# Kernel tuning notes

Measured on AMD Instinct MI355X. Metric: run time of the kernel, lower is better.

## Reference

```python
import jax, jax.numpy as jnp
import numpy as np

C_EM, H_EM, C_A = 256, 8, 32
S, R = 1024, 256
LN_EPS = 1e-5
MASK_BIAS = 1e9


def setup_inputs() -> dict:
    key = jax.random.key(0)
    ks = jax.random.split(key, 8)
    sc = 0.02
    m = jax.random.normal(ks[0], (S, R, C_EM), jnp.float32)
    # binary column mask (float mask in the original; int here so it is a constant)
    mask = (jax.random.uniform(ks[1], (S, R)) < 0.9).astype(jnp.int32)
    return {
        "m": m,
        "ln_g": jnp.ones((C_EM,), jnp.float32),
        "ln_b": jnp.zeros((C_EM,), jnp.float32),
        "w_q": jax.random.normal(ks[2], (C_EM, H_EM, C_A), jnp.float32) * sc,
        "w_k": jax.random.normal(ks[3], (C_EM, C_A), jnp.float32) * sc,
        "w_v": jax.random.normal(ks[4], (C_EM, C_A), jnp.float32) * sc,
        "w_g": jax.random.normal(ks[5], (C_EM, H_EM, C_A), jnp.float32) * sc,
        "b_g": jnp.zeros((H_EM, C_A), jnp.float32),
        "w_o": jax.random.normal(ks[6], (H_EM, C_A, C_EM), jnp.float32) * sc,
        "b_o": jnp.zeros((C_EM,), jnp.float32),
        "mask": mask,
    }


def reference(m, ln_g, ln_b, w_q, w_k, w_v, w_g, b_g, w_o, b_o, mask):
    maskf = mask.astype(m.dtype)  # [s, r]
    # LayerNorm over c_em (biased variance, eps=1e-5, torch default)
    mu = jnp.mean(m, axis=-1, keepdims=True)
    var = jnp.mean((m - mu) ** 2, axis=-1, keepdims=True)
    x = (m - mu) * jax.lax.rsqrt(var + LN_EPS) * ln_g + ln_b  # [s, r, c]
    # masked mean-pool over s -> per-column query
    q_pool = jnp.sum(x * maskf[..., None], axis=-3) / (jnp.sum(maskf, axis=-2)[..., None] + 1e-10)  # [r, c]
    Q = jnp.einsum('rc,chd->rhd', q_pool, w_q) * (1.0 / np.sqrt(C_A))  # [r, h, d]
    K = jnp.einsum('src,cd->srd', x, w_k)  # [s, r, d]
    V = jnp.einsum('src,cd->srd', x, w_v)  # [s, r, d]
    G = jax.nn.sigmoid(jnp.einsum('src,chd->srhd', x, w_g) + b_g)  # [s, r, h, d]
    bias = (maskf - 1.0) * MASK_BIAS  # [s, r]
    logits = jnp.einsum('rhd,srd->srh', Q, K) + bias[..., None]  # [s, r, h]
    A = jax.nn.softmax(logits, axis=-3)  # softmax over s
    O = jnp.einsum('srh,srd->rhd', A, V)  # [r, h, d]
    out = jnp.einsum('srhd,hdc->src', O[None, :, :, :] * G, w_o) + b_o  # [s, r, c]
    return out
```

## Files before the change

### kernel.cpp

```cpp
#include <hip/hip_runtime.h>
#include <math.h>

#define S_DIM 1024
#define R_DIM 256
#define C_DIM 256
#define SCALE 0.17677669529663687f

typedef short bf16x8 __attribute__((ext_vector_type(8)));
typedef float f32x4 __attribute__((ext_vector_type(4)));

__device__ __forceinline__ float wred(float v) {
#pragma unroll
  for (int m = 32; m >= 1; m >>= 1) v += __shfl_xor(v, m, 64);
  return v;
}

__device__ __forceinline__ short f2bf(float f) {
  union { float f; unsigned u; } v;
  v.f = f;
  unsigned r = v.u + 0x7fffu + ((v.u >> 16) & 1u);
  return (short)(r >> 16);
}

__device__ __forceinline__ float bf2f(short s) {
  union { unsigned u; float f; } v;
  v.u = ((unsigned)(unsigned short)s) << 16;
  return v.f;
}

__device__ __forceinline__ float fast_sigmoid_mul(float o, float gl) {
  return o * __builtin_amdgcn_rcpf(1.f + __expf(-gl));
}

__global__ __launch_bounds__(256)
void k0_prep(const float* __restrict__ w_g, const float* __restrict__ w_o,
             const float* __restrict__ w_k, const float* __restrict__ w_v,
             short* __restrict__ wgB, short* __restrict__ woB,
             short* __restrict__ wkvB) {
  const int id = blockIdx.x * 256 + threadIdx.x;
  if (id < 16384) {
    const int which = id >> 13;
    const int s = id & 8191;
    const int n = s & 255, g = (s >> 8) & 3, kb = s >> 10;
    const float* W = which ? w_o : w_g;
    short* Out = which ? woB : wgB;
#pragma unroll
    for (int j = 0; j < 8; ++j)
      Out[(((size_t)kb * 256 + n) * 4 + g) * 8 + j] =
          f2bf(W[(size_t)(kb * 32 + g * 8 + j) * 256 + n]);
  } else {
    const int s = id - 16384;
    const int n = s & 63, g = (s >> 6) & 3, kb = s >> 8;
    const float* W = (n < 32) ? w_k : w_v;
    const int nn = n & 31;
#pragma unroll
    for (int j = 0; j < 8; ++j)
      wkvB[(((size_t)kb * 64 + n) * 4 + g) * 8 + j] =
          f2bf(W[(size_t)(kb * 32 + g * 8 + j) * 32 + nn]);
  }
}

__global__ __launch_bounds__(256, 3)
void k1_ln_kv(const float* __restrict__ mIn, const float* __restrict__ ln_g,
              const float* __restrict__ ln_b, const short* __restrict__ wkvB,
              const int* __restrict__ mask,
              float* __restrict__ mu_ws, float* __restrict__ rs_ws,
              float* __restrict__ K_ws, float* __restrict__ V_ws,
              float* __restrict__ pool_ws) {
  __shared__ __align__(16) short A_lds[2048 * 8];
  __shared__ float mask_s[64];
  __shared__ float4 poolp[4][64];
  const int r  = blockIdx.y;
  const int s0 = blockIdx.x * 64;
  const int t  = threadIdx.x;

  if (t < 64) mask_s[t] = mask[(s0 + t) * R_DIM + r] ? 1.f : 0.f;

  {
    const int rw = t >> 2;
    const int q  = t & 3;
    const size_t p = (size_t)(s0 + rw) * R_DIM + r;
    const float* src = mIn + p * C_DIM + q * 64;
    float4 xv[16];
    float sum = 0.f, ssq = 0.f;
#pragma unroll
    for (int i = 0; i < 16; ++i) {
      xv[i] = *(const float4*)(src + i * 4);
      sum += xv[i].x + xv[i].y + xv[i].z + xv[i].w;
      ssq += xv[i].x * xv[i].x + xv[i].y * xv[i].y + xv[i].z * xv[i].z +
             xv[i].w * xv[i].w;
    }
    sum += __shfl_xor(sum, 1, 64); ssq += __shfl_xor(ssq, 1, 64);
    sum += __shfl_xor(sum, 2, 64); ssq += __shfl_xor(ssq, 2, 64);
    const float mu = sum * (1.f / 256.f);
    const float var = ssq * (1.f / 256.f) - mu * mu;
    const float rs = rsqrtf(var + 1e-5f);
    if (q == 0) { mu_ws[p] = mu; rs_ws[p] = rs; }

    const int gw = rw >> 4;
    const int lf0 = rw & 15;
#pragma unroll
    for (int kh = 0; kh < 2; ++kh) {
      const int kb = 2 * q + kh;
#pragma unroll
      for (int g = 0; g < 4; ++g) {
        const int lidx = kh * 32 + g * 8;
        const float4 a0 = xv[lidx >> 2], a1 = xv[(lidx >> 2) + 1];
        const float4 g0 = *(const float4*)(ln_g + kb * 32 + g * 8);
        const float4 g1 = *(const float4*)(ln_g + kb * 32 + g * 8 + 4);
        const float4 b0 = *(const float4*)(ln_b + kb * 32 + g * 8);
        const float4 b1 = *(const float4*)(ln_b + kb * 32 + g * 8 + 4);
        bf16x8 f;
        f[0] = f2bf((a0.x - mu) * rs * g0.x + b0.x);
        f[1] = f2bf((a0.y - mu) * rs * g0.y + b0.y);
        f[2] = f2bf((a0.z - mu) * rs * g0.z + b0.z);
        f[3] = f2bf((a0.w - mu) * rs * g0.w + b0.w);
        f[4] = f2bf((a1.x - mu) * rs * g1.x + b1.x);
        f[5] = f2bf((a1.y - mu) * rs * g1.y + b1.y);
        f[6] = f2bf((a1.z - mu) * rs * g1.z + b1.z);
        f[7] = f2bf((a1.w - mu) * rs * g1.w + b1.w);
        int byte = (((gw * 8 + kb) * 64 + lf0 + g * 16) << 4) ^ (((kb >> 1) & 3) << 5);
        *(bf16x8*)((char*)A_lds + byte) = f;
      }
    }
  }
  __syncthreads();

  {
    const int w = t >> 6, l = t & 63;
    const int lm = l & 15, g = l >> 4;
    f32x4 acc[4];
#pragma unroll
    for (int ni = 0; ni < 4; ++ni) acc[ni] = (f32x4){0.f, 0.f, 0.f, 0.f};
#pragma unroll
    for (int kb = 0; kb < 8; ++kb) {
      const int byte = (((w * 8 + kb) * 64 + l) << 4) ^ (((kb >> 1) & 3) << 5);
      const bf16x8 a = *(const bf16x8*)((char*)A_lds + byte);
      bf16x8 bfr[4];
#pragma unroll
      for (int ni = 0; ni < 4; ++ni)
        bfr[ni] = *(const bf16x8*)(wkvB + (((size_t)kb * 64 + lm + ni * 16) * 4 + g) * 8);
#pragma unroll
      for (int ni = 0; ni < 4; ++ni)
        acc[ni] = __builtin_amdgcn_mfma_f32_16x16x32_bf16(a, bfr[ni], acc[ni], 0, 0, 0);
    }
#pragma unroll
    for (int ni = 0; ni < 4; ++ni) {
      const int col = lm + ni * 16;
      float* Out = (col < 32) ? K_ws : V_ws;
      const int cc = col & 31;
#pragma unroll
      for (int reg = 0; reg < 4; ++reg) {
        const int s = s0 + w * 16 + g * 4 + reg;
        Out[((size_t)s * R_DIM + r) * 32 + cc] = acc[ni][reg];
      }
    }
  }

  {
    const int lc = t & 63;
    const int wq = t >> 6;
    const int kb = lc >> 3, g2 = (lc >> 1) & 3, bh = (lc & 1) * 4;
    float4 ps = make_float4(0.f, 0.f, 0.f, 0.f);
    for (int i = 0; i < 16; ++i) {
      const int rloc = (i + lc) & 15;
      const int byte =
          ((((wq * 8 + kb) * 64 + rloc + g2 * 16) << 4) + bh * 2) ^ (((kb >> 1) & 3) << 5);
      const short4 xb = *(const short4*)((char*)A_lds + byte);
      const float mk = mask_s[wq * 16 + rloc];
      ps.x += mk * bf2f(xb.x);
      ps.y += mk * bf2f(xb.y);
      ps.z += mk * bf2f(xb.z);
      ps.w += mk * bf2f(xb.w);
    }
    poolp[wq][lc] = ps;
  }
  __syncthreads();
  if (t < 64) {
    const float4 a = poolp[0][t], b = poolp[1][t], c = poolp[2][t], d = poolp[3][t];
    atomicAdd(&pool_ws[r * C_DIM + t * 4 + 0], a.x + b.x + c.x + d.x);
    atomicAdd(&pool_ws[r * C_DIM + t * 4 + 1], a.y + b.y + c.y + d.y);
    atomicAdd(&pool_ws[r * C_DIM + t * 4 + 2], a.z + b.z + c.z + d.z);
    atomicAdd(&pool_ws[r * C_DIM + t * 4 + 3], a.w + b.w + c.w + d.w);
  }
}

__global__ __launch_bounds__(256, 2)
void k2_q(const float* __restrict__ pool_ws, const int* __restrict__ mask,
          const float* __restrict__ w_q, float* __restrict__ Q_ws) {
  __shared__ float qp[256];
  __shared__ float wsum[4];
  const int r = blockIdx.x, t = threadIdx.x;
  int cnt = 0;
  for (int s = t; s < S_DIM; s += 256) cnt += mask[s * R_DIM + r];
  float cf = wred((float)cnt);
  if ((t & 63) == 0) wsum[t >> 6] = cf;
  __syncthreads();
  const float denom = wsum[0] + wsum[1] + wsum[2] + wsum[3] + 1e-10f;
  qp[t] = pool_ws[r * C_DIM + t] / denom;
  __syncthreads();
  float acc = 0.f;
  for (int c = 0; c < 256; ++c) acc += qp[c] * w_q[c * 256 + t];
  Q_ws[r * 256 + t] = acc * SCALE;
}

__global__ __launch_bounds__(256, 2)
void k3_attn(const float* __restrict__ K_ws, const float* __restrict__ V_ws,
             const int* __restrict__ mask, const float* __restrict__ Q_ws,
             float* __restrict__ O_ws) {
  __shared__ float q[256];
  __shared__ float lg[1024 * 9];
  __shared__ float kv[256 * 36];
  __shared__ float mh[8], inv[8];
  const int r = blockIdx.x, t = threadIdx.x;
  q[t] = Q_ws[r * 256 + t];

  for (int ch = 0; ch < 4; ++ch) {
    const int sb = ch * 256;
    __syncthreads();
    for (int f = t; f < 2048; f += 256) {
      const int sl = f >> 3, dq = f & 7;
      *(float4*)(kv + sl * 36 + dq * 4) =
          *(const float4*)(K_ws + ((size_t)(sb + sl) * R_DIM + r) * 32 + dq * 4);
    }
    __syncthreads();
    float kr[32];
#pragma unroll
    for (int dq = 0; dq < 8; ++dq)
      *(float4*)(kr + dq * 4) = *(float4*)(kv + t * 36 + dq * 4);
    const float bias = mask[(sb + t) * R_DIM + r] ? 0.f : -1e9f;
#pragma unroll
    for (int h = 0; h < 8; ++h) {
      float a = 0.f;
#pragma unroll
      for (int d = 0; d < 32; ++d) a += q[h * 32 + d] * kr[d];
      lg[(sb + t) * 9 + h] = a + bias;
    }
  }
  __syncthreads();
  {
    const int h = t >> 5, l32 = t & 31;
    float mx = -INFINITY;
    for (int k = 0; k < 32; ++k) mx = fmaxf(mx, lg[(l32 + 32 * k) * 9 + h]);
#pragma unroll
    for (int mk = 16; mk >= 1; mk >>= 1) mx = fmaxf(mx, __shfl_xor(mx, mk, 64));
    float sm = 0.f;
    for (int k = 0; k < 32; ++k) sm += __expf(lg[(l32 + 32 * k) * 9 + h] - mx);
#pragma unroll
    for (int mk = 16; mk >= 1; mk >>= 1) sm += __shfl_xor(sm, mk, 64);
    if (l32 == 0) { mh[h] = mx; inv[h] = 1.f / sm; }
  }
  __syncthreads();
  for (int f = t; f < 8192; f += 256) {
    const int s = f >> 3, h = f & 7;
    lg[s * 9 + h] = __expf(lg[s * 9 + h] - mh[h]) * inv[h];
  }
  const int h = t >> 5, d = t & 31;
  float o = 0.f;
  for (int ch = 0; ch < 4; ++ch) {
    const int sb = ch * 256;
    __syncthreads();
    for (int f = t; f < 2048; f += 256) {
      const int sl = f >> 3, dq = f & 7;
      *(float4*)(kv + sl * 36 + dq * 4) =
          *(const float4*)(V_ws + ((size_t)(sb + sl) * R_DIM + r) * 32 + dq * 4);
    }
    __syncthreads();
    for (int sl = 0; sl < 256; ++sl)
      o += lg[(sb + sl) * 9 + h] * kv[sl * 36 + d];
  }
  O_ws[r * 256 + t] = o;
}

__global__ __launch_bounds__(256, 4)
void k4_mfma(const float* __restrict__ mIn, const float* __restrict__ ln_g,
             const float* __restrict__ ln_b, const float* __restrict__ mu_ws,
             const float* __restrict__ rs_ws, const short* __restrict__ wgB,
             const float* __restrict__ b_g, const float* __restrict__ O_ws,
             const short* __restrict__ woB, const float* __restrict__ b_o,
             float* __restrict__ out) {
  __shared__ __align__(16) short A_lds[2048 * 8];
  const int t = threadIdx.x;
  const int p0 = blockIdx.x * 64;
  const int r0 = p0 & 255;
  const int l = t & 63;
  const int w = t >> 6;
  const int lm = l & 15;
  const int g = l >> 4;

  {
    const int row = w * 16 + lm;
    const size_t p = (size_t)(p0 + row);
    const float mu = mu_ws[p], rs = rs_ws[p];
    const float* mrow = mIn + p * 256 + g * 8;
    const float* gp = ln_g + g * 8;
    const float* bp = ln_b + g * 8;
#pragma unroll
    for (int kb = 0; kb < 8; ++kb) {
      const float4 m0 = *(const float4*)(mrow + kb * 32);
      const float4 m1 = *(const float4*)(mrow + kb * 32 + 4);
      const float4 g0 = *(const float4*)(gp + kb * 32);
      const float4 g1 = *(const float4*)(gp + kb * 32 + 4);
      const float4 b0 = *(const float4*)(bp + kb * 32);
      const float4 b1 = *(const float4*)(bp + kb * 32 + 4);
      bf16x8 xf;
      xf[0] = f2bf((m0.x - mu) * rs * g0.x + b0.x);
      xf[1] = f2bf((m0.y - mu) * rs * g0.y + b0.y);
      xf[2] = f2bf((m0.z - mu) * rs * g0.z + b0.z);
      xf[3] = f2bf((m0.w - mu) * rs * g0.w + b0.w);
      xf[4] = f2bf((m1.x - mu) * rs * g1.x + b1.x);
      xf[5] = f2bf((m1.y - mu) * rs * g1.y + b1.y);
      xf[6] = f2bf((m1.z - mu) * rs * g1.z + b1.z);
      xf[7] = f2bf((m1.w - mu) * rs * g1.w + b1.w);
      *(bf16x8*)(A_lds + ((w * 8 + kb) * 64 + l) * 8) = xf;
    }
  }
  __syncthreads();

  const int col = w * 64 + lm;
  f32x4 acc[4][4];

#pragma unroll
  for (int ni = 0; ni < 4; ++ni) {
    const float bg = b_g[col + ni * 16];
#pragma unroll
    for (int mi = 0; mi < 4; ++mi) acc[mi][ni] = (f32x4){bg, bg, bg, bg};
  }
#pragma unroll
  for (int kb = 0; kb < 8; ++kb) {
    bf16x8 a[4], bb[4];
#pragma unroll
    for (int mi = 0; mi < 4; ++mi)
      a[mi] = *(const bf16x8*)(A_lds + ((mi * 8 + kb) * 64 + l) * 8);
#pragma unroll
    for (int ni = 0; ni < 4; ++ni)
      bb[ni] = *(const bf16x8*)(wgB + (((size_t)kb * 256 + col + ni * 16) * 4 + g) * 8);
#pragma unroll
    for (int mi = 0; mi < 4; ++mi)
#pragma unroll
      for (int ni = 0; ni < 4; ++ni)
        acc[mi][ni] = __builtin_amdgcn_mfma_f32_16x16x32_bf16(a[mi], bb[ni], acc[mi][ni], 0, 0, 0);
  }
  __syncthreads();

#pragma unroll
  for (int mi = 0; mi < 4; ++mi) {
#pragma unroll
    for (int ni = 0; ni < 4; ++ni) {
      const int c2 = col + ni * 16;
      const int kb2 = c2 >> 5, g2 = (c2 >> 3) & 3, b2 = c2 & 7;
#pragma unroll
      for (int reg = 0; reg < 4; ++reg) {
        const int row = mi * 16 + g * 4 + reg;
        const float o = O_ws[(r0 + row) * 256 + c2];
        const float tv = fast_sigmoid_mul(o, acc[mi][ni][reg]);
        const int u = (mi * 8 + kb2) * 64 + (g * 4 + reg) + g2 * 16;
        const int byte = ((u << 4) ^ (((u >> 4) & 3) << 4)) + b2 * 2;
        *(short*)((char*)A_lds + byte) = f2bf(tv);
      }
    }
  }
  __syncthreads();

#pragma unroll
  for (int ni = 0; ni < 4; ++ni) {
    const float bo = b_o[col + ni * 16];
#pragma unroll
    for (int mi = 0; mi < 4; ++mi) acc[mi][ni] = (f32x4){bo, bo, bo, bo};
  }
#pragma unroll
  for (int kb = 0; kb < 8; ++kb) {
    bf16x8 a[4], bb[4];
#pragma unroll
    for (int mi = 0; mi < 4; ++mi) {
      const int u = (mi * 8 + kb) * 64 + l;
      const int byte = (u << 4) ^ (g << 4);
      a[mi] = *(const bf16x8*)((char*)A_lds + byte);
    }
#pragma unroll
    for (int ni = 0; ni < 4; ++ni)
      bb[ni] = *(const bf16x8*)(woB + (((size_t)kb * 256 + col + ni * 16) * 4 + g) * 8);
#pragma unroll
    for (int mi = 0; mi < 4; ++mi)
#pragma unroll
      for (int ni = 0; ni < 4; ++ni)
        acc[mi][ni] = __builtin_amdgcn_mfma_f32_16x16x32_bf16(a[mi], bb[ni], acc[mi][ni], 0, 0, 0);
  }

#pragma unroll
  for (int mi = 0; mi < 4; ++mi)
#pragma unroll
    for (int ni = 0; ni < 4; ++ni)
#pragma unroll
      for (int reg = 0; reg < 4; ++reg) {
        const int row = mi * 16 + g * 4 + reg;
        out[(size_t)(p0 + row) * 256 + col + ni * 16] = acc[mi][ni][reg];
      }
}

extern "C" void kernel_launch(void* const* d_in, const int* in_sizes, int n_in,
                              void* d_out, int out_size, void* d_ws, size_t ws_size,
                              hipStream_t stream) {
  const float* mIn  = (const float*)d_in[0];
  const float* ln_g = (const float*)d_in[1];
  const float* ln_b = (const float*)d_in[2];
  const float* w_q  = (const float*)d_in[3];
  const float* w_k  = (const float*)d_in[4];
  const float* w_v  = (const float*)d_in[5];
  const float* w_g  = (const float*)d_in[6];
  const float* b_g  = (const float*)d_in[7];
  const float* w_o  = (const float*)d_in[8];
  const float* b_o  = (const float*)d_in[9];
  const int*   mask = (const int*)d_in[10];
  float* outp = (float*)d_out;

  char* ws = (char*)d_ws;
  const size_t NP = (size_t)S_DIM * R_DIM;
  float* mu_ws   = (float*)ws;
  float* rs_ws   = mu_ws + NP;
  float* K_ws    = rs_ws + NP;
  float* V_ws    = K_ws + NP * 32;
  float* pool_ws = V_ws + NP * 32;
  float* Q_ws    = pool_ws + 65536;
  float* O_ws    = Q_ws + 65536;
  short* wgB     = (short*)(O_ws + 65536);
  short* woB     = wgB + 65536;
  short* wkvB    = woB + 65536;

  hipMemsetAsync(pool_ws, 0, 65536 * sizeof(float), stream);

  k0_prep<<<72, 256, 0, stream>>>(w_g, w_o, w_k, w_v, wgB, woB, wkvB);
  k1_ln_kv<<<dim3(S_DIM / 64, R_DIM), 256, 0, stream>>>(
      mIn, ln_g, ln_b, wkvB, mask, mu_ws, rs_ws, K_ws, V_ws, pool_ws);
  k2_q<<<R_DIM, 256, 0, stream>>>(pool_ws, mask, w_q, Q_ws);
  k3_attn<<<R_DIM, 256, 0, stream>>>(K_ws, V_ws, mask, Q_ws, O_ws);
  k4_mfma<<<dim3(S_DIM * R_DIM / 64), 256, 0, stream>>>(
      mIn, ln_g, ln_b, mu_ws, rs_ws, wgB, b_g, O_ws, woB, b_o, outp);
}
```

Baseline: 381.6 us.

## Fuse Q projection into attention kernel and prefetch weights in MFMA loops

Merges the per-column Q projection kernel into the attention kernel, so the mask is loaded once into registers and reused for both the count and the bias. This removes one launch and the Q workspace round trip. In the gating/output MFMA kernel, the B-operand weight fragments are now double-buffered in registers, loading the next k-block while the current one's MFMAs issue. The extra registers may affect occupancy.

```diff
diff --git a/kernel.cpp b/kernel.cpp
--- a/kernel.cpp
+++ b/kernel.cpp
@@ -186,34 +186,32 @@
 }
 
 __global__ __launch_bounds__(256, 2)
-void k2_q(const float* __restrict__ pool_ws, const int* __restrict__ mask,
-          const float* __restrict__ w_q, float* __restrict__ Q_ws) {
+void k3_attn(const float* __restrict__ K_ws, const float* __restrict__ V_ws,
+             const int* __restrict__ mask, const float* __restrict__ pool_ws,
+             const float* __restrict__ w_q, float* __restrict__ O_ws) {
+  __shared__ float q[256];
   __shared__ float qp[256];
-  __shared__ float wsum[4];
-  const int r = blockIdx.x, t = threadIdx.x;
-  int cnt = 0;
-  for (int s = t; s < S_DIM; s += 256) cnt += mask[s * R_DIM + r];
-  float cf = wred((float)cnt);
-  if ((t & 63) == 0) wsum[t >> 6] = cf;
-  __syncthreads();
-  const float denom = wsum[0] + wsum[1] + wsum[2] + wsum[3] + 1e-10f;
-  qp[t] = pool_ws[r * C_DIM + t] / denom;
-  __syncthreads();
-  float acc = 0.f;
-  for (int c = 0; c < 256; ++c) acc += qp[c] * w_q[c * 256 + t];
-  Q_ws[r * 256 + t] = acc * SCALE;
-}
-
-__global__ __launch_bounds__(256, 2)
-void k3_attn(const float* __restrict__ K_ws, const float* __restrict__ V_ws,
-             const int* __restrict__ mask, const float* __restrict__ Q_ws,
-             float* __restrict__ O_ws) {
-  __shared__ float q[256];
   __shared__ float lg[1024 * 9];
   __shared__ float kv[256 * 36];
   __shared__ float mh[8], inv[8];
+  __shared__ float wsum[4];
   const int r = blockIdx.x, t = threadIdx.x;
-  q[t] = Q_ws[r * 256 + t];
+
+  int mk[4];
+#pragma unroll
+  for (int ch = 0; ch < 4; ++ch) mk[ch] = mask[(ch * 256 + t) * R_DIM + r];
+  float cf = wred((float)(mk[0] + mk[1] + mk[2] + mk[3]));
+  if ((t & 63) == 0) wsum[t >> 6] = cf;
+  __syncthreads();
+  const float denom = wsum[0] + wsum[1] + wsum[2] + wsum[3] + 1e-10f;
+  qp[t] = pool_ws[r * C_DIM + t] / denom;
+  __syncthreads();
+  {
+    float qa = 0.f;
+    for (int c = 0; c < 256; ++c) qa += qp[c] * w_q[c * 256 + t];
+    q[t] = qa * SCALE;
+  }
+  __syncthreads();
 
   for (int ch = 0; ch < 4; ++ch) {
     const int sb = ch * 256;
@@ -228,7 +226,7 @@
 #pragma unroll
     for (int dq = 0; dq < 8; ++dq)
       *(float4*)(kr + dq * 4) = *(float4*)(kv + t * 36 + dq * 4);
-    const float bias = mask[(sb + t) * R_DIM + r] ? 0.f : -1e9f;
+    const float bias = mk[ch] ? 0.f : -1e9f;
 #pragma unroll
     for (int h = 0; h < 8; ++h) {
       float a = 0.f;
@@ -243,11 +241,11 @@
     float mx = -INFINITY;
     for (int k = 0; k < 32; ++k) mx = fmaxf(mx, lg[(l32 + 32 * k) * 9 + h]);
 #pragma unroll
-    for (int mk = 16; mk >= 1; mk >>= 1) mx = fmaxf(mx, __shfl_xor(mx, mk, 64));
+    for (int mkk = 16; mkk >= 1; mkk >>= 1) mx = fmaxf(mx, __shfl_xor(mx, mkk, 64));
     float sm = 0.f;
     for (int k = 0; k < 32; ++k) sm += __expf(lg[(l32 + 32 * k) * 9 + h] - mx);
 #pragma unroll
-    for (int mk = 16; mk >= 1; mk >>= 1) sm += __shfl_xor(sm, mk, 64);
+    for (int mkk = 16; mkk >= 1; mkk >>= 1) sm += __shfl_xor(sm, mkk, 64);
     if (l32 == 0) { mh[h] = mx; inv[h] = 1.f / sm; }
   }
   __syncthreads();
@@ -287,6 +285,12 @@
   const int w = t >> 6;
   const int lm = l & 15;
   const int g = l >> 4;
+  const int col = w * 64 + lm;
+
+  bf16x8 bb_c[4], bb_n[4];
+#pragma unroll
+  for (int ni = 0; ni < 4; ++ni)
+    bb_c[ni] = *(const bf16x8*)(wgB + (((size_t)0 * 256 + col + ni * 16) * 4 + g) * 8);
 
   {
     const int row = w * 16 + lm;
@@ -317,7 +321,6 @@
   }
   __syncthreads();
 
-  const int col = w * 64 + lm;
   f32x4 acc[4][4];
 
 #pragma unroll
@@ -328,19 +331,28 @@
   }
 #pragma unroll
   for (int kb = 0; kb < 8; ++kb) {
-    bf16x8 a[4], bb[4];
+    bf16x8 a[4];
 #pragma unroll
     for (int mi = 0; mi < 4; ++mi)
       a[mi] = *(const bf16x8*)(A_lds + ((mi * 8 + kb) * 64 + l) * 8);
-#pragma unroll
-    for (int ni = 0; ni < 4; ++ni)
-      bb[ni] = *(const bf16x8*)(wgB + (((size_t)kb * 256 + col + ni * 16) * 4 + g) * 8);
+    if (kb < 7) {
+#pragma unroll
+      for (int ni = 0; ni < 4; ++ni)
+        bb_n[ni] = *(const bf16x8*)(wgB +
+            (((size_t)(kb + 1) * 256 + col + ni * 16) * 4 + g) * 8);
+    }
 #pragma unroll
     for (int mi = 0; mi < 4; ++mi)
 #pragma unroll
       for (int ni = 0; ni < 4; ++ni)
-        acc[mi][ni] = __builtin_amdgcn_mfma_f32_16x16x32_bf16(a[mi], bb[ni], acc[mi][ni], 0, 0, 0);
-  }
+        acc[mi][ni] = __builtin_amdgcn_mfma_f32_16x16x32_bf16(a[mi], bb_c[ni], acc[mi][ni], 0, 0, 0);
+#pragma unroll
+    for (int ni = 0; ni < 4; ++ni) bb_c[ni] = bb_n[ni];
+  }
+
+#pragma unroll
+  for (int ni = 0; ni < 4; ++ni)
+    bb_c[ni] = *(const bf16x8*)(woB + (((size_t)0 * 256 + col + ni * 16) * 4 + g) * 8);
   __syncthreads();
 
 #pragma unroll
@@ -370,21 +382,25 @@
   }
 #pragma unroll
   for (int kb = 0; kb < 8; ++kb) {
-    bf16x8 a[4], bb[4];
+    bf16x8 a[4];
 #pragma unroll
     for (int mi = 0; mi < 4; ++mi) {
       const int u = (mi * 8 + kb) * 64 + l;
-      const int byte = (u << 4) ^ (g << 4);
-      a[mi] = *(const bf16x8*)((char*)A_lds + byte);
-    }
-#pragma unroll
-    for (int ni = 0; ni < 4; ++ni)
-      bb[ni] = *(const bf16x8*)(woB + (((size_t)kb * 256 + col + ni * 16) * 4 + g) * 8);
+      a[mi] = *(const bf16x8*)((char*)A_lds + ((u << 4) ^ (g << 4)));
+    }
+    if (kb < 7) {
+#pragma unroll
+      for (int ni = 0; ni < 4; ++ni)
+        bb_n[ni] = *(const bf16x8*)(woB +
+            (((size_t)(kb + 1) * 256 + col + ni * 16) * 4 + g) * 8);
+    }
 #pragma unroll
     for (int mi = 0; mi < 4; ++mi)
 #pragma unroll
       for (int ni = 0; ni < 4; ++ni)
-        acc[mi][ni] = __builtin_amdgcn_mfma_f32_16x16x32_bf16(a[mi], bb[ni], acc[mi][ni], 0, 0, 0);
+        acc[mi][ni] = __builtin_amdgcn_mfma_f32_16x16x32_bf16(a[mi], bb_c[ni], acc[mi][ni], 0, 0, 0);
+#pragma unroll
+    for (int ni = 0; ni < 4; ++ni) bb_c[ni] = bb_n[ni];
   }
 
 #pragma unroll
@@ -421,8 +437,7 @@
   float* K_ws    = rs_ws + NP;
   float* V_ws    = K_ws + NP * 32;
   float* pool_ws = V_ws + NP * 32;
-  float* Q_ws    = pool_ws + 65536;
-  float* O_ws    = Q_ws + 65536;
+  float* O_ws    = pool_ws + 65536;
   short* wgB     = (short*)(O_ws + 65536);
   short* woB     = wgB + 65536;
   short* wkvB    = woB + 65536;
@@ -432,8 +447,7 @@
   k0_prep<<<72, 256, 0, stream>>>(w_g, w_o, w_k, w_v, wgB, woB, wkvB);
   k1_ln_kv<<<dim3(S_DIM / 64, R_DIM), 256, 0, stream>>>(
       mIn, ln_g, ln_b, wkvB, mask, mu_ws, rs_ws, K_ws, V_ws, pool_ws);
-  k2_q<<<R_DIM, 256, 0, stream>>>(pool_ws, mask, w_q, Q_ws);
-  k3_attn<<<R_DIM, 256, 0, stream>>>(K_ws, V_ws, mask, Q_ws, O_ws);
+  k3_attn<<<R_DIM, 256, 0, stream>>>(K_ws, V_ws, mask, pool_ws, w_q, O_ws);
   k4_mfma<<<dim3(S_DIM * R_DIM / 64), 256, 0, stream>>>(
       mIn, ln_g, ln_b, mu_ws, rs_ws, wgB, b_g, O_ws, woB, b_o, outp);
 }
```

After: 395.9 us. 3.8% more time.

## Split column attention into parallel logits, AV and normalize kernels with bf16 K/V

Applied to the files above, without the earlier changes.

Replaces the single per-column attention kernel, which had only 256 blocks, with three kernels. One computes exp(logits) over a grid spread along s and column and accumulates softmax denominators with atomics. One computes partial AV products per 256-row chunk, and one sums the partials and normalizes. K and V are now written by the LN kernel as bf16 in a column-major [r][s][d] layout to halve traffic and make per-column reads contiguous. The softmax drops max subtraction, which risks overflow for large logits, and adds an exp-score buffer plus extra launches.

```diff
diff --git a/kernel.cpp b/kernel.cpp
--- a/kernel.cpp
+++ b/kernel.cpp
@@ -65,7 +65,7 @@
               const float* __restrict__ ln_b, const short* __restrict__ wkvB,
               const int* __restrict__ mask,
               float* __restrict__ mu_ws, float* __restrict__ rs_ws,
-              float* __restrict__ K_ws, float* __restrict__ V_ws,
+              short* __restrict__ Kt, short* __restrict__ Vt,
               float* __restrict__ pool_ws) {
   __shared__ __align__(16) short A_lds[2048 * 8];
   __shared__ float mask_s[64];
@@ -147,12 +147,12 @@
 #pragma unroll
     for (int ni = 0; ni < 4; ++ni) {
       const int col = lm + ni * 16;
-      float* Out = (col < 32) ? K_ws : V_ws;
+      short* Out = (col < 32) ? Kt : Vt;
       const int cc = col & 31;
 #pragma unroll
       for (int reg = 0; reg < 4; ++reg) {
         const int s = s0 + w * 16 + g * 4 + reg;
-        Out[((size_t)s * R_DIM + r) * 32 + cc] = acc[ni][reg];
+        Out[((size_t)r * 1024 + s) * 32 + cc] = f2bf(acc[ni][reg]);
       }
     }
   }
@@ -204,72 +204,83 @@
   Q_ws[r * 256 + t] = acc * SCALE;
 }
 
-__global__ __launch_bounds__(256, 2)
-void k3_attn(const float* __restrict__ K_ws, const float* __restrict__ V_ws,
-             const int* __restrict__ mask, const float* __restrict__ Q_ws,
-             float* __restrict__ O_ws) {
+__global__ __launch_bounds__(256, 4)
+void k3e_logits(const short* __restrict__ Kt, const float* __restrict__ Q_ws,
+                const int* __restrict__ mask, float* __restrict__ E_ws,
+                float* __restrict__ D_ws) {
   __shared__ float q[256];
-  __shared__ float lg[1024 * 9];
-  __shared__ float kv[256 * 36];
-  __shared__ float mh[8], inv[8];
+  const int r = blockIdx.y, s0 = blockIdx.x * 64;
+  const int t = threadIdx.x, w = t >> 6, l = t & 63;
+  q[t] = Q_ws[r * 256 + t];
+  __syncthreads();
+  const int s = s0 + l;
+  const short* kp = Kt + ((size_t)r * 1024 + s) * 32;
+  bf16x8 kr[4];
+#pragma unroll
+  for (int i = 0; i < 4; ++i) kr[i] = *(const bf16x8*)(kp + i * 8);
+  const int mk = mask[s * R_DIM + r];
+  float e01[2];
+#pragma unroll
+  for (int hh = 0; hh < 2; ++hh) {
+    const int h = 2 * w + hh;
+    float a = 0.f;
+#pragma unroll
+    for (int i = 0; i < 4; ++i)
+#pragma unroll
+      for (int j = 0; j < 8; ++j)
+        a += q[h * 32 + i * 8 + j] * bf2f(kr[i][j]);
+    e01[hh] = mk ? __expf(a) : 0.f;
+    E_ws[((size_t)r * 8 + h) * 1024 + s] = e01[hh];
+  }
+  const float d0 = wred(e01[0]);
+  const float d1 = wred(e01[1]);
+  if (l == 0) {
+    atomicAdd(&D_ws[r * 8 + 2 * w + 0], d0);
+    atomicAdd(&D_ws[r * 8 + 2 * w + 1], d1);
+  }
+}
+
+__global__ __launch_bounds__(256, 4)
+void k3b_av(const short* __restrict__ Vt, const float* __restrict__ E_ws,
+            float* __restrict__ Npart) {
+  __shared__ float A_s[8 * 256];
+  __shared__ __align__(16) short V_s[256 * 32];
+  const int ch = blockIdx.x, r = blockIdx.y;
+  const int t = threadIdx.x;
+  const int sb = ch * 256;
+#pragma unroll
+  for (int h = 0; h < 8; ++h)
+    A_s[h * 256 + t] = E_ws[((size_t)r * 8 + h) * 1024 + sb + t];
+  {
+    const short* vp = Vt + ((size_t)r * 1024 + sb) * 32;
+#pragma unroll
+    for (int i = 0; i < 4; ++i) {
+      const int u = i * 256 + t;
+      *(bf16x8*)(V_s + u * 8) = *(const bf16x8*)(vp + u * 8);
+    }
+  }
+  __syncthreads();
+  const int h = t >> 5, d = t & 31;
+  const float* ap = A_s + h * 256;
+  float o = 0.f;
+  for (int s4 = 0; s4 < 256; s4 += 4) {
+    const float4 a4 = *(const float4*)(ap + s4);
+    o += a4.x * bf2f(V_s[(s4 + 0) * 32 + d]);
+    o += a4.y * bf2f(V_s[(s4 + 1) * 32 + d]);
+    o += a4.z * bf2f(V_s[(s4 + 2) * 32 + d]);
+    o += a4.w * bf2f(V_s[(s4 + 3) * 32 + d]);
+  }
+  Npart[(size_t)ch * 65536 + r * 256 + t] = o;
+}
+
+__global__ __launch_bounds__(256)
+void k3c_norm(const float* __restrict__ Npart, const float* __restrict__ D_ws,
+              float* __restrict__ O_ws) {
   const int r = blockIdx.x, t = threadIdx.x;
-  q[t] = Q_ws[r * 256 + t];
-
-  for (int ch = 0; ch < 4; ++ch) {
-    const int sb = ch * 256;
-    __syncthreads();
-    for (int f = t; f < 2048; f += 256) {
-      const int sl = f >> 3, dq = f & 7;
-      *(float4*)(kv + sl * 36 + dq * 4) =
-          *(const float4*)(K_ws + ((size_t)(sb + sl) * R_DIM + r) * 32 + dq * 4);
-    }
-    __syncthreads();
-    float kr[32];
-#pragma unroll
-    for (int dq = 0; dq < 8; ++dq)
-      *(float4*)(kr + dq * 4) = *(float4*)(kv + t * 36 + dq * 4);
-    const float bias = mask[(sb + t) * R_DIM + r] ? 0.f : -1e9f;
-#pragma unroll
-    for (int h = 0; h < 8; ++h) {
-      float a = 0.f;
-#pragma unroll
-      for (int d = 0; d < 32; ++d) a += q[h * 32 + d] * kr[d];
-      lg[(sb + t) * 9 + h] = a + bias;
-    }
-  }
-  __syncthreads();
-  {
-    const int h = t >> 5, l32 = t & 31;
-    float mx = -INFINITY;
-    for (int k = 0; k < 32; ++k) mx = fmaxf(mx, lg[(l32 + 32 * k) * 9 + h]);
-#pragma unroll
-    for (int mk = 16; mk >= 1; mk >>= 1) mx = fmaxf(mx, __shfl_xor(mx, mk, 64));
-    float sm = 0.f;
-    for (int k = 0; k < 32; ++k) sm += __expf(lg[(l32 + 32 * k) * 9 + h] - mx);
-#pragma unroll
-    for (int mk = 16; mk >= 1; mk >>= 1) sm += __shfl_xor(sm, mk, 64);
-    if (l32 == 0) { mh[h] = mx; inv[h] = 1.f / sm; }
-  }
-  __syncthreads();
-  for (int f = t; f < 8192; f += 256) {
-    const int s = f >> 3, h = f & 7;
-    lg[s * 9 + h] = __expf(lg[s * 9 + h] - mh[h]) * inv[h];
-  }
-  const int h = t >> 5, d = t & 31;
-  float o = 0.f;
-  for (int ch = 0; ch < 4; ++ch) {
-    const int sb = ch * 256;
-    __syncthreads();
-    for (int f = t; f < 2048; f += 256) {
-      const int sl = f >> 3, dq = f & 7;
-      *(float4*)(kv + sl * 36 + dq * 4) =
-          *(const float4*)(V_ws + ((size_t)(sb + sl) * R_DIM + r) * 32 + dq * 4);
-    }
-    __syncthreads();
-    for (int sl = 0; sl < 256; ++sl)
-      o += lg[(sb + sl) * 9 + h] * kv[sl * 36 + d];
-  }
-  O_ws[r * 256 + t] = o;
+  const int idx = r * 256 + t;
+  const float n = Npart[idx] + Npart[65536 + idx] + Npart[131072 + idx] +
+                  Npart[196608 + idx];
+  O_ws[idx] = n / (D_ws[r * 8 + (t >> 5)] + 1e-30f);
 }
 
 __global__ __launch_bounds__(256, 4)
@@ -414,26 +425,32 @@
   const int*   mask = (const int*)d_in[10];
   float* outp = (float*)d_out;
 
-  char* ws = (char*)d_ws;
+  float* ws = (float*)d_ws;
   const size_t NP = (size_t)S_DIM * R_DIM;
-  float* mu_ws   = (float*)ws;
+  float* mu_ws   = ws;
   float* rs_ws   = mu_ws + NP;
-  float* K_ws    = rs_ws + NP;
-  float* V_ws    = K_ws + NP * 32;
-  float* pool_ws = V_ws + NP * 32;
-  float* Q_ws    = pool_ws + 65536;
-  float* O_ws    = Q_ws + 65536;
+  short* Kt      = (short*)(rs_ws + NP);
+  short* Vt      = Kt + (size_t)256 * 1024 * 32;
+  float* pool_ws = (float*)(Vt + (size_t)256 * 1024 * 32);
+  float* D_ws    = pool_ws + 65536;
+  float* Q_ws    = D_ws + 2048;
+  float* E_ws    = Q_ws + 65536;
+  float* Npart   = E_ws + 2097152;
+  float* O_ws    = Npart + 262144;
   short* wgB     = (short*)(O_ws + 65536);
   short* woB     = wgB + 65536;
   short* wkvB    = woB + 65536;
 
-  hipMemsetAsync(pool_ws, 0, 65536 * sizeof(float), stream);
+  hipMemsetAsync(pool_ws, 0, (65536 + 2048) * sizeof(float), stream);
 
   k0_prep<<<72, 256, 0, stream>>>(w_g, w_o, w_k, w_v, wgB, woB, wkvB);
   k1_ln_kv<<<dim3(S_DIM / 64, R_DIM), 256, 0, stream>>>(
-      mIn, ln_g, ln_b, wkvB, mask, mu_ws, rs_ws, K_ws, V_ws, pool_ws);
+      mIn, ln_g, ln_b, wkvB, mask, mu_ws, rs_ws, Kt, Vt, pool_ws);
   k2_q<<<R_DIM, 256, 0, stream>>>(pool_ws, mask, w_q, Q_ws);
-  k3_attn<<<R_DIM, 256, 0, stream>>>(K_ws, V_ws, mask, Q_ws, O_ws);
+  k3e_logits<<<dim3(S_DIM / 64, R_DIM), 256, 0, stream>>>(
+      Kt, Q_ws, mask, E_ws, D_ws);
+  k3b_av<<<dim3(4, R_DIM), 256, 0, stream>>>(Vt, E_ws, Npart);
+  k3c_norm<<<R_DIM, 256, 0, stream>>>(Npart, D_ws, O_ws);
   k4_mfma<<<dim3(S_DIM * R_DIM / 64), 256, 0, stream>>>(
       mIn, ln_g, ln_b, mu_ws, rs_ws, wgB, b_g, O_ws, woB, b_o, outp);
 }
```

Result: faster. 368.3 us (-3.5%).
